# Performance work log

Measured on AMD Instinct MI355X. Metric: run time of the kernel, lower is better.

The kernel has to match this reference:

```python
import jax, jax.numpy as jnp
import numpy as np

N = 200      # nodes (fixed by Linear(200,100) on x.T)
E = 8000     # edges
NFEAT, NHID, NCLASS = 8192, 2048, 512


def _cheb_conv(x, edge_index, edge_weight, W, b):
    """PyG ChebConv (K=3, sym norm, lambda_max=2): L_hat = -D^{-1/2} A D^{-1/2}.
    T0 = x, T1 = L_hat x, T2 = 2 L_hat T1 - T0; out = sum_k T_k @ W[k] + b."""
    row, col = edge_index[0], edge_index[1]
    deg = jax.ops.segment_sum(edge_weight, row, num_segments=N)
    safe = jnp.where(deg > 0, deg, 1.0)
    dinv = jnp.where(deg > 0, 1.0 / jnp.sqrt(safe), 0.0)
    norm = -dinv[row] * edge_weight * dinv[col]  # [E]

    def lap(z):  # messages from source j=row to target i=col
        return jax.ops.segment_sum(norm[:, None] * z[row], col, num_segments=N)

    T1 = lap(x)
    T2 = 2.0 * lap(T1) - x
    return x @ W[0] + T1 @ W[1] + T2 @ W[2] + b


def _forward_single(x, ei, ew, W1, b1, W2, b2):
    h = jax.nn.relu(_cheb_conv(x, ei, ew, W1, b1))
    # dropout is identity in eval mode
    return _cheb_conv(h, ei, ew, W2, b2)  # [N, NCLASS]


def _classifier(z, Wc1, bc1, Wc2, bc2, Wc3, bc3):
    h = jax.nn.relu(z @ Wc1.T + bc1)
    h = jax.nn.relu(h @ Wc2.T + bc2)
    return h @ Wc3.T + bc3  # [NCLASS, 1]


def setup_inputs() -> dict:
    key = jax.random.key(0)
    ks = jax.random.split(key, 12)
    inp = {
        'x1': jax.random.normal(ks[0], (N, NFEAT), jnp.float32),
        'edge_index1': jax.random.randint(ks[1], (2, E), 0, N, jnp.int64),
        'edge_attr1': jax.random.uniform(ks[2], (E,), jnp.float32),
        'x2': jax.random.normal(ks[3], (N, NFEAT), jnp.float32),
        'edge_index2': jax.random.randint(ks[4], (2, E), 0, N, jnp.int64),
        'edge_attr2': jax.random.uniform(ks[5], (E,), jnp.float32),
        'W1': jax.random.normal(ks[6], (3, NFEAT, NHID), jnp.float32) * (NFEAT ** -0.5),
        'b1': jnp.zeros((NHID,), jnp.float32),
        'W2': jax.random.normal(ks[7], (3, NHID, NCLASS), jnp.float32) * (NHID ** -0.5),
        'b2': jnp.zeros((NCLASS,), jnp.float32),
        'Wc1': jax.random.normal(ks[8], (100, 200), jnp.float32) * (200 ** -0.5),
        'bc1': jnp.zeros((100,), jnp.float32),
        'Wc2': jax.random.normal(ks[9], (50, 100), jnp.float32) * (100 ** -0.5),
        'bc2': jnp.zeros((50,), jnp.float32),
        'Wc3': jax.random.normal(ks[10], (1, 50), jnp.float32) * (50 ** -0.5),
        'bc3': jnp.zeros((1,), jnp.float32),
    }
    return inp


def reference(x1, edge_index1, edge_attr1, x2, edge_index2, edge_attr2,
              W1, b1, W2, b2, Wc1, bc1, Wc2, bc2, Wc3, bc3):
    o1 = _forward_single(x1, edge_index1, edge_attr1, W1, b1, W2, b2)
    o2 = _forward_single(x2, edge_index2, edge_attr2, W1, b1, W2, b2)
    out1 = _classifier(o1.T, Wc1, bc1, Wc2, bc2, Wc3, bc3)  # [NCLASS, 1]
    out2 = _classifier(o2.T, Wc1, bc1, Wc2, bc2, Wc3, bc3)
    return out1, out2
```

## Files before the change

kernel.cpp:

```cpp
#include <hip/hip_runtime.h>

typedef __attribute__((ext_vector_type(8))) short short8;
typedef __attribute__((ext_vector_type(4))) float f32x4;
typedef __attribute__((ext_vector_type(2))) float f32x2;
typedef __attribute__((ext_vector_type(4))) unsigned int u32x4;

#define NNODES 200
#define NEDGE  8000
#define NF1    8192
#define NH     2048
#define NCL    512
#define K1     24576
#define K2     6144
#define MR     448
#define MV     400
#define PV     400
#define KC1    16
#define BK1    1536
#define KC2    16
#define BK2    384

#define OFF_P1  0ull
#define SZ_P1   (16ull*PV*NH*4)
#define OFF_P2  (OFF_P1 + SZ_P1)
#define SZ_P2   (16ull*PV*NCL*4)
#define OFF_A1  (OFF_P2 + SZ_P2)
#define SZ_A1   ((unsigned long long)MR*K1*2)
#define OFF_A2  (OFF_A1 + SZ_A1)
#define SZ_A2   ((unsigned long long)MR*K2*2)
#define OFF_DEG (OFF_A2 + SZ_A2)
#define OFF_LD  (OFF_DEG + 2048)
#define OFF_LL  (OFF_LD + 320000ull)
#define OFF_Z   OFF_P1

static __device__ __forceinline__ unsigned short f2bf(float f) {
  unsigned int u = __float_as_uint(f);
  unsigned int r = (u + 0x7fffu + ((u >> 16) & 1u)) >> 16;
  return (unsigned short)r;
}
static __device__ __forceinline__ unsigned packbf(float a, float b) {
  return (unsigned)f2bf(a) | ((unsigned)f2bf(b) << 16);
}

__global__ void k_zero(f32x4* p1, int n1, f32x4* p2, int n2, f32x4* p3, int n3) {
  int i = blockIdx.x * 256 + threadIdx.x;
  f32x4 z = {0.f, 0.f, 0.f, 0.f};
  if (i < n1) p1[i] = z;
  i -= n1;
  if (i >= 0 && i < n2) p2[i] = z;
  i -= n2;
  if (i >= 0 && i < n3) p3[i] = z;
}

__global__ void k_deg(const int* __restrict__ ei1, const float* __restrict__ ew1,
                      const int* __restrict__ ei2, const float* __restrict__ ew2,
                      float* __restrict__ deg) {
  int e = blockIdx.x * 256 + threadIdx.x;
  if (e >= 2 * NEDGE) return;
  int g = e / NEDGE, k = e % NEDGE;
  const int* ei = g ? ei2 : ei1;
  const float* ew = g ? ew2 : ew1;
  atomicAdd(deg + g * NNODES + ei[k], ew[k]);
}

__global__ void k_buildL(const int* __restrict__ ei1, const float* __restrict__ ew1,
                         const int* __restrict__ ei2, const float* __restrict__ ew2,
                         const float* __restrict__ deg, float* __restrict__ Ld) {
  int e = blockIdx.x * 256 + threadIdx.x;
  if (e >= 2 * NEDGE) return;
  int g = e / NEDGE, k = e % NEDGE;
  const int* ei = g ? ei2 : ei1;
  const float* ew = g ? ew2 : ew1;
  int r = ei[k], c = ei[NEDGE + k];
  float dr = deg[g * NNODES + r], dc = deg[g * NNODES + c];
  float ir = dr > 0.f ? 1.0f / sqrtf(dr) : 0.f;
  float ic = dc > 0.f ? 1.0f / sqrtf(dc) : 0.f;
  float nrm = -ir * ew[k] * ic;
  atomicAdd(Ld + ((size_t)g * NNODES + c) * NNODES + r, nrm);
}

__global__ void k_LL(const float* __restrict__ Ld, unsigned short* __restrict__ LLb) {
  int b = blockIdx.x;
  int g = b / NNODES, i = b % NNODES;
  __shared__ float Lr[NNODES];
  const float* Lg = Ld + (size_t)g * NNODES * NNODES;
  int t = threadIdx.x;
  if (t < NNODES) Lr[t] = Lg[i * NNODES + t];
  __syncthreads();
  if (t < NNODES) {
    float acc = 0.f;
    for (int k = 0; k < NNODES; ++k) acc = fmaf(Lr[k], Lg[k * NNODES + t], acc);
    unsigned short* LLg = LLb + (size_t)g * MR * 224;
    LLg[(size_t)i * 224 + t] = f2bf(Lr[t]);
    LLg[(size_t)(NNODES + i) * 224 + t] = f2bf(2.f * acc - (i == t ? 1.f : 0.f));
  }
}

__global__ void k_t0(const float* __restrict__ x1, const float* __restrict__ x2,
                     unsigned short* __restrict__ A1) {
  int gid = blockIdx.x * 256 + threadIdx.x;
  int row = gid / (NF1 / 8);
  int c8 = (gid % (NF1 / 8)) * 8;
  const float* xp = (row < NNODES ? x1 + (size_t)row * NF1
                                  : x2 + (size_t)(row - NNODES) * NF1) + c8;
  f32x4 a = *(const f32x4*)xp;
  f32x4 b = *(const f32x4*)(xp + 4);
  u32x4 o;
  o[0] = packbf(a[0], a[1]);
  o[1] = packbf(a[2], a[3]);
  o[2] = packbf(b[0], b[1]);
  o[3] = packbf(b[2], b[3]);
  *(u32x4*)(A1 + (size_t)row * K1 + c8) = o;
}

__global__ __launch_bounds__(256, 1)
void k_abuild(const unsigned short* __restrict__ LLb, const unsigned short* __restrict__ Asrc,
              unsigned short* __restrict__ Adst, const int Nf, const int Ka) {
  __shared__ __align__(16) unsigned short XF[7][4][64][8];
  const int g = blockIdx.x & 1;
  const int nt = blockIdx.x >> 1;
  const int nbase = nt * 64;
  const int t = threadIdx.x;

  #pragma unroll
  for (int it = 0; it < 14; ++it) {
    const int pos = it * 256 + t;
    const int j = pos >> 4;
    const int n4 = (pos & 15) * 4;
    unsigned long long v = 0ull;
    if (j < NNODES)
      v = *(const unsigned long long*)(Asrc + (size_t)(g * NNODES + j) * Ka + nbase + n4);
    const int ks = j >> 5, kg = (j >> 3) & 3, jj = j & 7;
    #pragma unroll
    for (int e = 0; e < 4; ++e) {
      const int nn = n4 + e;
      XF[ks][nn >> 4][(nn & 15) + 16 * kg][jj] = (unsigned short)(v >> (16 * e));
    }
  }
  __syncthreads();

  const int w = t >> 6, lane = t & 63;
  const int lm = lane & 15, lk8 = (lane >> 4) * 8;
  f32x4 acc[7][4];
  #pragma unroll
  for (int i = 0; i < 7; ++i)
    #pragma unroll
    for (int j = 0; j < 4; ++j) acc[i][j] = (f32x4){0.f, 0.f, 0.f, 0.f};

  const unsigned short* LLg = LLb + (size_t)g * MR * 224;
  #pragma unroll
  for (int ks = 0; ks < 7; ++ks) {
    short8 bfr[4];
    #pragma unroll
    for (int nf = 0; nf < 4; ++nf) bfr[nf] = *(const short8*)&XF[ks][nf][lane][0];
    short8 af[7];
    #pragma unroll
    for (int mf = 0; mf < 7; ++mf)
      af[mf] = *(const short8*)(LLg + (size_t)(w * 112 + mf * 16 + lm) * 224 + ks * 32 + lk8);
    #pragma unroll
    for (int mf = 0; mf < 7; ++mf)
      #pragma unroll
      for (int nf = 0; nf < 4; ++nf)
        acc[mf][nf] = __builtin_amdgcn_mfma_f32_16x16x32_bf16(af[mf], bfr[nf], acc[mf][nf], 0, 0, 0);
  }

  const int lr4 = (lane >> 4) * 4;
  #pragma unroll
  for (int mf = 0; mf < 7; ++mf) {
    #pragma unroll
    for (int ri = 0; ri < 4; ++ri) {
      const int m = w * 112 + mf * 16 + lr4 + ri;
      if (m < MV) {
        const int drow = g * NNODES + (m < NNODES ? m : m - NNODES);
        const size_t dbase = (size_t)drow * Ka + (m < NNODES ? Nf : 2 * Nf) + nbase + lm;
        #pragma unroll
        for (int nf = 0; nf < 4; ++nf)
          Adst[dbase + nf * 16] = f2bf(acc[mf][nf][ri]);
      }
    }
  }
}

template <int BN, int KA>
__global__ __launch_bounds__(512, 2)
void k_gemm(const float* __restrict__ W, const unsigned short* __restrict__ A,
            float* __restrict__ P, const int Nn, const int BK) {
  constexpr int NF = BN / 16;
  constexpr int NFW = BN / 32;
  constexpr int CW = BN / 16;
  constexpr int ABUF = MR * 128;
  constexpr int BSTRIDE = NF * 1024;
  constexpr int WBUF = 2 * BSTRIDE;
  __shared__ __align__(16) unsigned short Atile[2 * MR * 64];
  __shared__ __align__(16) unsigned short Wt[2 * NF * 1024];

  const int t = threadIdx.x;
  const int w = t >> 6, lane = t & 63;
  const int wm = w >> 1, wn = w & 1;
  const int lm = lane & 15;
  const int l4 = lane >> 4;
  const int kc = blockIdx.x & 15;
  const int nt = blockIdx.x >> 4;
  const int kbase = kc * BK;
  const int nbase = nt * BN;
  const int nks = BK >> 6;

  const int arow0 = t >> 3;
  const int agb = ((t * 16) & 127) ^ ((arow0 & 7) << 4);
  const char* Ab = (const char*)A + (size_t)kbase * 2 + (size_t)arow0 * (KA * 2) + agb;
  const size_t CSTEP = (size_t)64 * KA * 2;

  const int kk0 = (t >> 4) * 2;
  const int colb = (t & 15) * CW;
  const float* Wg = W + (size_t)(kbase + kk0) * Nn + nbase + colb;
  int offWl[CW];
  {
    const int ks0 = kk0 >> 5, kg0 = (kk0 >> 3) & 3, jj1 = (kk0 & 7) >> 1;
    #pragma unroll
    for (int e = 0; e < CW; ++e) {
      const int nn = colb + e;
      const int nf = nn >> 4;
      const int ln = ((nn & 15) + 16 * kg0) ^ (nf & 3);
      offWl[e] = ((ks0 * NF + nf) * 64 + ln) * 4 + jj1;
    }
  }

  const int aBase = (wm * 112 + lm) * 128 + ((l4 * 16) ^ ((lm & 7) << 4));
  int bAddr[NFW];
  #pragma unroll
  for (int nf = 0; nf < NFW; ++nf) {
    const int nfg = wn * NFW + nf;
    bAddr[nf] = nfg * 1024 + (lane ^ (nfg & 3)) * 16;
  }

  f32x4 acc[7][NFW];
  #pragma unroll
  for (int i = 0; i < 7; ++i)
    #pragma unroll
    for (int j = 0; j < NFW; ++j) acc[i][j] = (f32x4){0.f, 0.f, 0.f, 0.f};

  u32x4 areg[7];
  f32x4 w0a, w0b, w1a, w1b;
  f32x2 w0s, w1s;

  auto loadW = [&](int kt) {
    const float* p = Wg + (size_t)kt * 64 * Nn;
    if constexpr (BN == 128) {
      w0a = __builtin_nontemporal_load((const f32x4*)p);
      w0b = __builtin_nontemporal_load((const f32x4*)(p + 4));
      w1a = __builtin_nontemporal_load((const f32x4*)(p + Nn));
      w1b = __builtin_nontemporal_load((const f32x4*)(p + Nn + 4));
    } else {
      w0s = __builtin_nontemporal_load((const f32x2*)p);
      w1s = __builtin_nontemporal_load((const f32x2*)(p + Nn));
    }
  };
  auto loadA = [&](int kt) {
    #pragma unroll
    for (int c = 0; c < 7; ++c)
      areg[c] = *(const u32x4*)(Ab + c * CSTEP + (size_t)kt * 128);
  };
  auto storeA = [&](int buf) {
    #pragma unroll
    for (int c = 0; c < 7; ++c)
      *(u32x4*)((char*)Atile + buf * ABUF + c * 8192 + t * 16) = areg[c];
  };
  auto storeW = [&](int buf) {
    unsigned* w32 = (unsigned*)Wt + buf * (WBUF / 4);
    #pragma unroll
    for (int e = 0; e < CW; ++e) {
      float lo, hi;
      if constexpr (BN == 128) {
        lo = (e < 4) ? w0a[e & 3] : w0b[e & 3];
        hi = (e < 4) ? w1a[e & 3] : w1b[e & 3];
      } else {
        lo = w0s[e & 1];
        hi = w1s[e & 1];
      }
      w32[offWl[e]] = packbf(lo, hi);
    }
  };

  loadW(0);
  loadA(0);
  storeA(0);
  storeW(0);
  __syncthreads();

  for (int kt = 0; kt < nks; ++kt) {
    const int buf = kt & 1;
    const bool more = (kt + 1 < nks);
    if (more) loadW(kt + 1);

    #pragma unroll
    for (int ks = 0; ks < 2; ++ks) {
      short8 bfr[NFW];
      #pragma unroll
      for (int nf = 0; nf < NFW; ++nf)
        bfr[nf] = *(const short8*)((const char*)Wt + buf * WBUF + bAddr[nf] + ks * BSTRIDE);
      const int abx = (aBase ^ (ks * 64)) + buf * ABUF;
      short8 af[7];
      #pragma unroll
      for (int mf = 0; mf < 7; ++mf)
        af[mf] = *(const short8*)((const char*)Atile + abx + mf * 2048);
      #pragma unroll
      for (int mf = 0; mf < 7; ++mf)
        #pragma unroll
        for (int nf = 0; nf < NFW; ++nf)
          acc[mf][nf] = __builtin_amdgcn_mfma_f32_16x16x32_bf16(af[mf], bfr[nf], acc[mf][nf], 0, 0, 0);
      if (ks == 0 && more) loadA(kt + 1);
    }

    if (more) {
      storeA(buf ^ 1);
      storeW(buf ^ 1);
    }
    __syncthreads();
  }

  float* Pk = P + ((size_t)kc * PV) * Nn + nbase;
  #pragma unroll
  for (int mf = 0; mf < 7; ++mf) {
    const int row0 = wm * 112 + mf * 16 + l4 * 4;
    #pragma unroll
    for (int ri = 0; ri < 4; ++ri) {
      const int row = row0 + ri;
      if (row < MV) {
        #pragma unroll
        for (int nf = 0; nf < NFW; ++nf) {
          const int col = (wn * NFW + nf) * 16 + lm;
          __builtin_nontemporal_store(acc[mf][nf][ri], Pk + (size_t)row * Nn + col);
        }
      }
    }
  }
}

__global__ void k_ep1(const float* __restrict__ P1, const float* __restrict__ b1,
                      unsigned short* __restrict__ A2) {
  int gid = blockIdx.x * 256 + threadIdx.x;
  int row = gid / (NH / 4);
  int c = (gid % (NH / 4)) * 4;
  f32x4 s = {0.f, 0.f, 0.f, 0.f};
  #pragma unroll
  for (int kc = 0; kc < KC1; ++kc)
    s += __builtin_nontemporal_load((const f32x4*)(P1 + ((size_t)kc * PV + row) * NH + c));
  const f32x4 b = *(const f32x4*)(b1 + c);
  unsigned long long pack = 0;
  #pragma unroll
  for (int i = 0; i < 4; ++i) {
    float v = s[i] + b[i];
    pack |= (unsigned long long)f2bf(v > 0.f ? v : 0.f) << (16 * i);
  }
  *(unsigned long long*)(A2 + (size_t)row * K2 + c) = pack;
}

__global__ __launch_bounds__(256)
void k_zsum(const float* __restrict__ P2, const float* __restrict__ b2,
            float* __restrict__ zt) {
  __shared__ float tile[8][264];
  const int b = blockIdx.x;
  const int g = b / 50;
  const int r2 = b % 50;
  const int j0 = (r2 >> 1) * 8;
  const int ch = (r2 & 1) * 256;
  const int t = threadIdx.x;
  const int j = t >> 5;
  const int c0 = (t & 31) * 8;
  const int row = g * NNODES + j0 + j;

  #pragma unroll
  for (int ci = 0; ci < 2; ++ci) {
    const int c = c0 + ci * 4;
    f32x4 s = *(const f32x4*)(b2 + ch + c);
    #pragma unroll
    for (int kc = 0; kc < KC2; ++kc)
      s += __builtin_nontemporal_load((const f32x4*)(P2 + ((size_t)kc * PV + row) * NCL + ch + c));
    *(f32x4*)&tile[j][c] = s;
  }
  __syncthreads();

  f32x4 lo, hi;
  #pragma unroll
  for (int e = 0; e < 4; ++e) { lo[e] = tile[e][t]; hi[e] = tile[4 + e][t]; }
  float* zr = zt + ((size_t)g * NCL + ch + t) * 200 + j0;
  *(f32x4*)zr = lo;
  *(f32x4*)(zr + 4) = hi;
}

__global__ __launch_bounds__(256)
void k_cls2(const float* __restrict__ zt,
            const float* __restrict__ Wc1, const float* __restrict__ bc1,
            const float* __restrict__ Wc2, const float* __restrict__ bc2,
            const float* __restrict__ Wc3, const float* __restrict__ bc3,
            float* __restrict__ outp) {
  __shared__ float zs[4][200];
  __shared__ float h1s[4][100];
  __shared__ float h2s[4][50];
  const int g = blockIdx.x >> 7;
  const int t = threadIdx.x;
  const int w = t >> 6, lane = t & 63;
  const int r = (blockIdx.x & 127) * 4 + w;

  const float* zr = zt + ((size_t)g * NCL + r) * 200;
  #pragma unroll
  for (int i = 0; i < 4; ++i) {
    const int idx = i * 64 + lane;
    if (idx < 200) zs[w][idx] = zr[idx];
  }
  __syncthreads();

  {
    const int c0 = lane;
    const int c1 = lane + 64;
    const int c1m = (c1 < 100) ? c1 : 99;
    float a0 = bc1[c0 < 100 ? c0 : 99];
    float a1 = bc1[c1m];
    const float* w0 = Wc1 + c0 * 200;
    const float* w1 = Wc1 + c1m * 200;
    #pragma unroll 8
    for (int j = 0; j < 200; ++j) {
      const float zv = zs[w][j];
      a0 = fmaf(zv, w0[j], a0);
      a1 = fmaf(zv, w1[j], a1);
    }
    if (c0 < 100) h1s[w][c0] = a0 > 0.f ? a0 : 0.f;
    if (c1 < 100) h1s[w][c1] = a1 > 0.f ? a1 : 0.f;
  }
  __syncthreads();

  {
    const int c2 = (lane < 50) ? lane : 49;
    float b = bc2[c2];
    const float* w2 = Wc2 + c2 * 100;
    #pragma unroll 10
    for (int c = 0; c < 100; ++c) b = fmaf(h1s[w][c], w2[c], b);
    if (lane < 50) h2s[w][lane] = b > 0.f ? b : 0.f;
  }
  __syncthreads();

  {
    float v = (lane < 50) ? h2s[w][lane] * Wc3[lane] : 0.f;
    #pragma unroll
    for (int off = 32; off >= 1; off >>= 1) v += __shfl_down(v, off);
    if (lane == 0) outp[g * NCL + r] = v + bc3[0];
  }
}

extern "C" void kernel_launch(void* const* d_in, const int* in_sizes, int n_in,
                              void* d_out, int out_size, void* d_ws, size_t ws_size,
                              hipStream_t stream) {
  const float* x1  = (const float*)d_in[0];
  const int*   ei1 = (const int*)d_in[1];
  const float* ea1 = (const float*)d_in[2];
  const float* x2  = (const float*)d_in[3];
  const int*   ei2 = (const int*)d_in[4];
  const float* ea2 = (const float*)d_in[5];
  const float* W1  = (const float*)d_in[6];
  const float* b1  = (const float*)d_in[7];
  const float* W2  = (const float*)d_in[8];
  const float* b2  = (const float*)d_in[9];
  const float* Wc1 = (const float*)d_in[10];
  const float* bc1 = (const float*)d_in[11];
  const float* Wc2 = (const float*)d_in[12];
  const float* bc2 = (const float*)d_in[13];
  const float* Wc3 = (const float*)d_in[14];
  const float* bc3 = (const float*)d_in[15];
  float* outp = (float*)d_out;

  char* ws = (char*)d_ws;
  float*          P1  = (float*)(ws + OFF_P1);
  float*          P2  = (float*)(ws + OFF_P2);
  unsigned short* A1  = (unsigned short*)(ws + OFF_A1);
  unsigned short* A2  = (unsigned short*)(ws + OFF_A2);
  float*          deg = (float*)(ws + OFF_DEG);
  float*          Ld  = (float*)(ws + OFF_LD);
  unsigned short* LLb = (unsigned short*)(ws + OFF_LL);
  float*          zt  = (float*)(ws + OFF_Z);

  k_zero<<<897, 256, 0, stream>>>(
      (f32x4*)(ws + OFF_DEG), 45216,
      (f32x4*)(ws + OFF_A1 + (size_t)MV * K1 * 2), 147456,
      (f32x4*)(ws + OFF_A2 + (size_t)MV * K2 * 2), 36864);

  k_deg<<<63, 256, 0, stream>>>(ei1, ea1, ei2, ea2, deg);
  k_buildL<<<63, 256, 0, stream>>>(ei1, ea1, ei2, ea2, deg, Ld);
  k_LL<<<400, 256, 0, stream>>>(Ld, LLb);
  k_t0<<<1600, 256, 0, stream>>>(x1, x2, A1);
  k_abuild<<<(NF1 / 64) * 2, 256, 0, stream>>>(LLb, A1, A1, NF1, K1);
  k_gemm<128, K1><<<KC1 * (NH / 128), 512, 0, stream>>>(W1, A1, P1, NH, BK1);
  k_ep1<<<800, 256, 0, stream>>>(P1, b1, A2);
  k_abuild<<<(NH / 64) * 2, 256, 0, stream>>>(LLb, A2, A2, NH, K2);
  k_gemm<32, K2><<<KC2 * (NCL / 32), 512, 0, stream>>>(W2, A2, P2, NCL, BK2);
  k_zsum<<<100, 256, 0, stream>>>(P2, b2, zt);
  k_cls2<<<256, 256, 0, stream>>>(zt, Wc1, bc1, Wc2, bc2, Wc3, bc3, outp);
}
```

Baseline: 177.0 us.

## Retile first GEMM to BN=64 with half the split-K and stage classifier weights in LDS

```diff
diff --git a/kernel.cpp b/kernel.cpp
--- a/kernel.cpp
+++ b/kernel.cpp
@@ -15,15 +15,15 @@
 #define MR     448
 #define MV     400
 #define PV     400
-#define KC1    16
-#define BK1    1536
+#define KC1    8
+#define BK1    3072
 #define KC2    16
 #define BK2    384
 
 #define OFF_P1  0ull
-#define SZ_P1   (16ull*PV*NH*4)
+#define SZ_P1   ((unsigned long long)KC1*PV*NH*4)
 #define OFF_P2  (OFF_P1 + SZ_P1)
-#define SZ_P2   (16ull*PV*NCL*4)
+#define SZ_P2   ((unsigned long long)KC2*PV*NCL*4)
 #define OFF_A1  (OFF_P2 + SZ_P2)
 #define SZ_A1   ((unsigned long long)MR*K1*2)
 #define OFF_A2  (OFF_A1 + SZ_A1)
@@ -181,7 +181,7 @@
   }
 }
 
-template <int BN, int KA>
+template <int BN, int KA, int KC>
 __global__ __launch_bounds__(512, 2)
 void k_gemm(const float* __restrict__ W, const unsigned short* __restrict__ A,
             float* __restrict__ P, const int Nn, const int BK) {
@@ -199,8 +199,8 @@
   const int wm = w >> 1, wn = w & 1;
   const int lm = lane & 15;
   const int l4 = lane >> 4;
-  const int kc = blockIdx.x & 15;
-  const int nt = blockIdx.x >> 4;
+  const int kc = blockIdx.x % KC;
+  const int nt = blockIdx.x / KC;
   const int kbase = kc * BK;
   const int nbase = nt * BN;
   const int nks = BK >> 6;
@@ -250,6 +250,9 @@
       w0b = __builtin_nontemporal_load((const f32x4*)(p + 4));
       w1a = __builtin_nontemporal_load((const f32x4*)(p + Nn));
       w1b = __builtin_nontemporal_load((const f32x4*)(p + Nn + 4));
+    } else if constexpr (BN == 64) {
+      w0a = __builtin_nontemporal_load((const f32x4*)p);
+      w1a = __builtin_nontemporal_load((const f32x4*)(p + Nn));
     } else {
       w0s = __builtin_nontemporal_load((const f32x2*)p);
       w1s = __builtin_nontemporal_load((const f32x2*)(p + Nn));
@@ -273,6 +276,9 @@
       if constexpr (BN == 128) {
         lo = (e < 4) ? w0a[e & 3] : w0b[e & 3];
         hi = (e < 4) ? w1a[e & 3] : w1b[e & 3];
+      } else if constexpr (BN == 64) {
+        lo = w0a[e & 3];
+        hi = w1a[e & 3];
       } else {
         lo = w0s[e & 1];
         hi = w1s[e & 1];
@@ -394,14 +400,24 @@
             const float* __restrict__ Wc2, const float* __restrict__ bc2,
             const float* __restrict__ Wc3, const float* __restrict__ bc3,
             float* __restrict__ outp) {
+  __shared__ float W1s[100 * 201];
+  __shared__ float W2s[50 * 101];
   __shared__ float zs[4][200];
-  __shared__ float h1s[4][100];
-  __shared__ float h2s[4][50];
+  __shared__ float h1s[4][104];
+  __shared__ float h2s[4][56];
   const int g = blockIdx.x >> 7;
   const int t = threadIdx.x;
   const int w = t >> 6, lane = t & 63;
   const int r = (blockIdx.x & 127) * 4 + w;
 
+  for (int i = t; i < 20000; i += 256) {
+    const int c = i / 200, j = i - c * 200;
+    W1s[c * 201 + j] = Wc1[i];
+  }
+  for (int i = t; i < 5000; i += 256) {
+    const int c = i / 100, j = i - c * 100;
+    W2s[c * 101 + j] = Wc2[i];
+  }
   const float* zr = zt + ((size_t)g * NCL + r) * 200;
   #pragma unroll
   for (int i = 0; i < 4; ++i) {
@@ -411,20 +427,17 @@
   __syncthreads();
 
   {
-    const int c0 = lane;
     const int c1 = lane + 64;
     const int c1m = (c1 < 100) ? c1 : 99;
-    float a0 = bc1[c0 < 100 ? c0 : 99];
+    float a0 = bc1[lane];
     float a1 = bc1[c1m];
-    const float* w0 = Wc1 + c0 * 200;
-    const float* w1 = Wc1 + c1m * 200;
-    #pragma unroll 8
+    #pragma unroll 4
     for (int j = 0; j < 200; ++j) {
       const float zv = zs[w][j];
-      a0 = fmaf(zv, w0[j], a0);
-      a1 = fmaf(zv, w1[j], a1);
-    }
-    if (c0 < 100) h1s[w][c0] = a0 > 0.f ? a0 : 0.f;
+      a0 = fmaf(zv, W1s[lane * 201 + j], a0);
+      a1 = fmaf(zv, W1s[c1m * 201 + j], a1);
+    }
+    h1s[w][lane] = a0 > 0.f ? a0 : 0.f;
     if (c1 < 100) h1s[w][c1] = a1 > 0.f ? a1 : 0.f;
   }
   __syncthreads();
@@ -432,9 +445,8 @@
   {
     const int c2 = (lane < 50) ? lane : 49;
     float b = bc2[c2];
-    const float* w2 = Wc2 + c2 * 100;
-    #pragma unroll 10
-    for (int c = 0; c < 100; ++c) b = fmaf(h1s[w][c], w2[c], b);
+    #pragma unroll 4
+    for (int c = 0; c < 100; ++c) b = fmaf(h1s[w][c], W2s[c2 * 101 + c], b);
     if (lane < 50) h2s[w][lane] = b > 0.f ? b : 0.f;
   }
   __syncthreads();
@@ -488,10 +500,10 @@
   k_LL<<<400, 256, 0, stream>>>(Ld, LLb);
   k_t0<<<1600, 256, 0, stream>>>(x1, x2, A1);
   k_abuild<<<(NF1 / 64) * 2, 256, 0, stream>>>(LLb, A1, A1, NF1, K1);
-  k_gemm<128, K1><<<KC1 * (NH / 128), 512, 0, stream>>>(W1, A1, P1, NH, BK1);
+  k_gemm<64, K1, KC1><<<KC1 * (NH / 64), 512, 0, stream>>>(W1, A1, P1, NH, BK1);
   k_ep1<<<800, 256, 0, stream>>>(P1, b1, A2);
   k_abuild<<<(NH / 64) * 2, 256, 0, stream>>>(LLb, A2, A2, NH, K2);
-  k_gemm<32, K2><<<KC2 * (NCL / 32), 512, 0, stream>>>(W2, A2, P2, NCL, BK2);
+  k_gemm<32, K2, KC2><<<KC2 * (NCL / 32), 512, 0, stream>>>(W2, A2, P2, NCL, BK2);
   k_zsum<<<100, 256, 0, stream>>>(P2, b2, zt);
   k_cls2<<<256, 256, 0, stream>>>(zt, Wc1, bc1, Wc2, bc2, Wc3, bc3, outp);
 }
```

New measurement: 181.3 us. 2.4% more time.
